# Performance work log

Measured on AMD Instinct MI355X. Metric: run time of the kernel, lower is better.

## Reference

```python
import jax, jax.numpy as jnp
import numpy as np

NUM_CLASSES = 9
TEMP = 0.1
ALPHA = 0.99
EPS = 1e-12  # F.normalize default eps


def _l2norm(x, axis=-1):
    n = jnp.linalg.norm(x, axis=axis, keepdims=True)
    return x / jnp.maximum(n, EPS)


def setup_inputs() -> dict:
    key = jax.random.key(0)
    k1, k2, k3, k4, k5 = jax.random.split(key, 5)
    B, D, h, w = 4, 768, 128, 128
    return {
        "cls_score": jax.random.normal(k1, (B, NUM_CLASSES, h, w), dtype=jnp.float32),
        "label": jax.random.randint(k2, (B, 4 * h, 4 * w), 0, NUM_CLASSES, dtype=jnp.int64),
        "gt_lucas": jax.random.randint(k3, (B, 4 * h, 4 * w), 0, NUM_CLASSES, dtype=jnp.int64),
        "features": jax.random.normal(k4, (B, D, h, w), dtype=jnp.float32),
        "prototypes": jax.random.uniform(k5, (NUM_CLASSES, D), dtype=jnp.float32),
    }


def reference(cls_score, label, gt_lucas, features, prototypes):
    B, D, h, w = features.shape
    # so the masked gathers reduce to a full flatten (static shapes).
    corine = label[:, ::4, ::4].reshape(-1)          # [N]
    lucas = gt_lucas[:, ::4, ::4].reshape(-1)        # [N] (mask trivially all valid)
    feats = jnp.transpose(features, (0, 2, 3, 1)).reshape(-1, D)  # [N, D]
    N = feats.shape[0]
    # note: original indexes corine labels under the lucas mask (mask all-true here)
    labels_lucas = corine
    labels_corine = jnp.where(corine == 7, 6, corine)
    # per-class EMA prototype update (unique(labels_lucas) == arange(9) by construction;
    # compute_ema detaches the new mean)
    sums = jax.ops.segment_sum(feats, labels_lucas, num_segments=NUM_CLASSES)      # [C, D]
    counts = jax.ops.segment_sum(jnp.ones((N,), feats.dtype), labels_lucas,
                                 num_segments=NUM_CLASSES)                          # [C]
    means = jax.lax.stop_gradient(sums / counts[:, None])
    protos = ALPHA * means + (1.0 - ALPHA) * prototypes
    protos = _l2norm(protos, axis=-1)                # F.normalize over feature dim
    logits = protos @ feats.T                        # [C, N]
    prot_feat = _l2norm(logits, axis=-1) / TEMP      # normalize each class row over N
    prot_feat = prot_feat.at[2].set((labels_corine == 2).astype(prot_feat.dtype))
    E = jnp.exp(prot_feat)                           # [C, N]
    A1 = E[labels_corine, jnp.arange(N)]             # [N]
    A2 = E.sum(axis=0)                               # [N]
    return jnp.mean(-jnp.log(A1 / A2))
```

## Files before the change

kernel.cpp:

```cpp
#include <hip/hip_runtime.h>
#include <math.h>

#define NCLS 9
#define DIM 768
#define NPIX 65536

#define OFF_LAB     ((size_t)0)
#define OFF_HIST    ((size_t)65536)
#define OFF_SUMS    ((size_t)74752)
#define OFF_SUMSQ   ((size_t)102400)
#define OFF_LOSS    ((size_t)102464)
#define OFF_DONE    ((size_t)102480)
#define OFF_LOGITS  ((size_t)139392)

__device__ __forceinline__ float waveReduceSum(float v) {
#pragma unroll
  for (int off = 32; off > 0; off >>= 1) v += __shfl_down(v, off, 64);
  return v;
}

__global__ void k0_lab(const int* __restrict__ label, unsigned char* __restrict__ lab,
                       int* __restrict__ hist, float* __restrict__ sumsq,
                       float* __restrict__ lossacc, unsigned int* __restrict__ done) {
  __shared__ int h[NCLS];
  int tid = threadIdx.x;
  if (tid < NCLS) h[tid] = 0;
  __syncthreads();
  int n = blockIdx.x * 256 + tid;
  int b = n >> 14, r = (n >> 7) & 127, cc = n & 127;
  int c = label[b * 262144 + r * 2048 + cc * 4];
  lab[n] = (unsigned char)c;
  atomicAdd(&h[c], 1);
  if (blockIdx.x == 0) {
    if (tid < 16) sumsq[tid] = 0.f;
    else if (tid == 16) lossacc[0] = 0.f;
    else if (tid == 17) done[0] = 0u;
  }
  __syncthreads();
  if (tid < NCLS) hist[blockIdx.x * NCLS + tid] = h[tid];
}

__global__ void k1_segsum(const float4* __restrict__ feat4, const uchar4* __restrict__ lab4,
                          float* __restrict__ sums) {
  int d = blockIdx.x;
  int tid = threadIdx.x;
  float acc[NCLS];
#pragma unroll
  for (int k = 0; k < NCLS; ++k) acc[k] = 0.f;
  for (int b = 0; b < 4; ++b) {
    const float4* fp = feat4 + (size_t)(b * DIM + d) * 4096;
    const uchar4* lp = lab4 + b * 4096;
#pragma unroll 4
    for (int i = 0; i < 16; ++i) {
      int p = tid + i * 256;
      float4 f = fp[p];
      uchar4 l = lp[p];
      int lx = l.x, ly = l.y, lz = l.z, lw = l.w;
#pragma unroll
      for (int k = 0; k < NCLS; ++k) {
        acc[k] += (lx == k) ? f.x : 0.f;
        acc[k] += (ly == k) ? f.y : 0.f;
        acc[k] += (lz == k) ? f.z : 0.f;
        acc[k] += (lw == k) ? f.w : 0.f;
      }
    }
  }
  __shared__ float red[4][NCLS];
#pragma unroll
  for (int k = 0; k < NCLS; ++k) acc[k] = waveReduceSum(acc[k]);
  int lane = tid & 63, w = tid >> 6;
  if (lane == 0) {
#pragma unroll
    for (int k = 0; k < NCLS; ++k) red[w][k] = acc[k];
  }
  __syncthreads();
  if (tid < NCLS)
    sums[tid * DIM + d] = red[0][tid] + red[1][tid] + red[2][tid] + red[3][tid];
}

__global__ void __launch_bounds__(1024, 8) k3_fused(const float* __restrict__ sums,
                                                    const int* __restrict__ hist,
                                                    const float* __restrict__ proto,
                                                    const float* __restrict__ feat,
                                                    float* __restrict__ logits,
                                                    float* __restrict__ sumsq) {
  __shared__ float pl[DIM * 12];
  __shared__ float cpart[32][NCLS];
  __shared__ float cnt[NCLS];
  __shared__ float red12[12][NCLS];
  __shared__ float invn[NCLS];
  __shared__ float red2[2][NCLS];
  int tid = threadIdx.x;

  if (tid < 288) {
    int c = tid % NCLS, g = tid / NCLS;
    int s = 0;
#pragma unroll
    for (int j = 0; j < 8; ++j) s += hist[(g * 8 + j) * NCLS + c];
    cpart[g][c] = (float)s;
  }
  __syncthreads();
  if (tid < NCLS) {
    float s = 0.f;
#pragma unroll
    for (int g = 0; g < 32; ++g) s += cpart[g][tid];
    cnt[tid] = s;
  }
  __syncthreads();

  float v[NCLS];
  if (tid < DIM) {
#pragma unroll
    for (int c = 0; c < NCLS; ++c)
      v[c] = 0.99f * (sums[c * DIM + tid] / cnt[c]) + 0.01f * proto[c * DIM + tid];
    int lane = tid & 63, w = tid >> 6;
#pragma unroll
    for (int c = 0; c < NCLS; ++c) {
      float q = waveReduceSum(v[c] * v[c]);
      if (lane == 0) red12[w][c] = q;
    }
  }
  __syncthreads();
  if (tid < NCLS) {
    float t = 0.f;
#pragma unroll
    for (int w2 = 0; w2 < 12; ++w2) t += red12[w2][tid];
    invn[tid] = 1.f / fmaxf(sqrtf(t), 1e-12f);
  }
  __syncthreads();
  if (tid < DIM) {
#pragma unroll
    for (int c = 0; c < NCLS; ++c) pl[tid * 12 + c] = v[c] * invn[c];
  }
  __syncthreads();

  int grp = tid >> 7, g = tid & 127;
  int n0 = blockIdx.x * 256;
  int b = n0 >> 14, ppb = n0 & 16383;
  const float* fr = feat + ((size_t)(b * DIM + grp * 96)) * 16384 + ppb + g;
  const float* pp = pl + (size_t)grp * 96 * 12;
  float a[NCLS][2];
#pragma unroll
  for (int c = 0; c < NCLS; ++c) { a[c][0] = 0.f; a[c][1] = 0.f; }

#pragma unroll 2
  for (int dd = 0; dd < 96; ++dd) {
    float f0 = fr[0], f1 = fr[128];
    float4 q0 = *(const float4*)pp;
    float4 q1 = *(const float4*)(pp + 4);
    float q8 = pp[8];
    float pcs[NCLS] = {q0.x, q0.y, q0.z, q0.w, q1.x, q1.y, q1.z, q1.w, q8};
#pragma unroll
    for (int c = 0; c < NCLS; ++c) {
      a[c][0] += pcs[c] * f0;
      a[c][1] += pcs[c] * f1;
    }
    fr += 16384;
    pp += 12;
  }
  __syncthreads();

  if (grp >= 4) {
    float* rp = pl + (size_t)(grp - 4) * 2304 + g;
#pragma unroll
    for (int c = 0; c < NCLS; ++c) {
      rp[c * 256] = a[c][0];
      rp[c * 256 + 128] = a[c][1];
    }
  }
  __syncthreads();
  if (grp < 4) {
    const float* rp = pl + (size_t)grp * 2304 + g;
#pragma unroll
    for (int c = 0; c < NCLS; ++c) {
      a[c][0] += rp[c * 256];
      a[c][1] += rp[c * 256 + 128];
    }
  }
  __syncthreads();
  if (grp >= 1 && grp < 4) {
    float* rp = pl + (size_t)(grp - 1) * 2304 + g;
#pragma unroll
    for (int c = 0; c < NCLS; ++c) {
      rp[c * 256] = a[c][0];
      rp[c * 256 + 128] = a[c][1];
    }
  }
  __syncthreads();
  if (grp == 0) {
#pragma unroll
    for (int q = 0; q < 3; ++q) {
      const float* rp = pl + (size_t)q * 2304 + g;
#pragma unroll
      for (int c = 0; c < NCLS; ++c) {
        a[c][0] += rp[c * 256];
        a[c][1] += rp[c * 256 + 128];
      }
    }
    float ss[NCLS];
#pragma unroll
    for (int c = 0; c < NCLS; ++c) {
      logits[(size_t)c * NPIX + n0 + g] = a[c][0];
      logits[(size_t)c * NPIX + n0 + 128 + g] = a[c][1];
      ss[c] = waveReduceSum(a[c][0] * a[c][0] + a[c][1] * a[c][1]);
    }
    int lane = tid & 63, w = tid >> 6;
    if (lane == 0) {
#pragma unroll
      for (int c = 0; c < NCLS; ++c) red2[w][c] = ss[c];
    }
  }
  __syncthreads();
  if (tid < NCLS) atomicAdd(&sumsq[tid], red2[0][tid] + red2[1][tid]);
}

__global__ void k5_loss(const float4* __restrict__ logits4, const uchar4* __restrict__ lab4,
                        const float* __restrict__ sumsq, float* __restrict__ lossacc,
                        unsigned int* __restrict__ done, float* __restrict__ out) {
  int t = blockIdx.x * 256 + threadIdx.x;
  int tid = threadIdx.x;
  float scale[NCLS];
#pragma unroll
  for (int c = 0; c < NCLS; ++c) scale[c] = 10.f / fmaxf(sqrtf(sumsq[c]), 1e-12f);
  float arr[NCLS][4];
#pragma unroll
  for (int c = 0; c < NCLS; ++c) {
    float4 v = logits4[(size_t)c * 16384 + t];
    arr[c][0] = v.x; arr[c][1] = v.y; arr[c][2] = v.z; arr[c][3] = v.w;
  }
  uchar4 lb = lab4[t];
  int lv[4] = {lb.x, lb.y, lb.z, lb.w};
  float lsum = 0.f;
#pragma unroll
  for (int j = 0; j < 4; ++j) {
    int l = lv[j];
    int lc = (l == 7) ? 6 : l;
    float sumE = 0.f, picked = 0.f;
#pragma unroll
    for (int c = 0; c < NCLS; ++c) {
      float pf = (c == 2) ? ((lc == 2) ? 1.f : 0.f) : arr[c][j] * scale[c];
      sumE += __expf(pf);
      picked += (c == lc) ? pf : 0.f;
    }
    lsum += __logf(sumE) - picked;
  }
  lsum = waveReduceSum(lsum);
  __shared__ float red[4];
  int lane = tid & 63, w = tid >> 6;
  if (lane == 0) red[w] = lsum;
  __syncthreads();
  if (tid == 0) {
    atomicAdd(lossacc, red[0] + red[1] + red[2] + red[3]);
    __threadfence();
    unsigned int ticket = atomicAdd(done, 1u);
    if (ticket == gridDim.x - 1) {
      __threadfence();
      float total = __hip_atomic_load(lossacc, __ATOMIC_ACQUIRE, __HIP_MEMORY_SCOPE_AGENT);
      out[0] = total * (1.f / (float)NPIX);
    }
  }
}

extern "C" void kernel_launch(void* const* d_in, const int* in_sizes, int n_in,
                              void* d_out, int out_size, void* d_ws, size_t ws_size,
                              hipStream_t stream) {
  const int* label = (const int*)d_in[1];
  const float* feat = (const float*)d_in[3];
  const float* proto = (const float*)d_in[4];
  char* ws = (char*)d_ws;
  unsigned char* lab = (unsigned char*)(ws + OFF_LAB);
  int* hist = (int*)(ws + OFF_HIST);
  float* sums = (float*)(ws + OFF_SUMS);
  float* sumsq = (float*)(ws + OFF_SUMSQ);
  float* lossacc = (float*)(ws + OFF_LOSS);
  unsigned int* done = (unsigned int*)(ws + OFF_DONE);
  float* logits = (float*)(ws + OFF_LOGITS);

  k0_lab<<<NPIX / 256, 256, 0, stream>>>(label, lab, hist, sumsq, lossacc, done);
  k1_segsum<<<DIM, 256, 0, stream>>>((const float4*)feat, (const uchar4*)lab, sums);
  k3_fused<<<NPIX / 256, 1024, 0, stream>>>(sums, hist, proto, feat, logits, sumsq);
  k5_loss<<<64, 256, 0, stream>>>((const float4*)logits, (const uchar4*)lab, sumsq, lossacc,
                                  done, (float*)d_out);
}
```

Baseline: 102.0 us.

## Split prototype normalization into a single-block kernel and read protos from global

The prototype EMA and L2 normalization used to be recomputed redundantly in each of the 256 blocks of the fused logits kernel. That work now runs once in a single-block kernel that writes a transposed, normalized prototype table to the workspace. The logits kernel reads prototypes directly from global or cache with a wave-uniform group index, and its unroll factor goes from 2 to 4. The cost is an extra kernel launch plus a serialized single-block step, and per-iteration prototype reads now go to global memory instead of LDS.

Result: slower. 110.0 us (+7.9%).

```diff
diff --git a/kernel.cpp b/kernel.cpp
--- a/kernel.cpp
+++ b/kernel.cpp
@@ -11,6 +11,7 @@
 #define OFF_SUMSQ   ((size_t)102400)
 #define OFF_LOSS    ((size_t)102464)
 #define OFF_DONE    ((size_t)102480)
+#define OFF_PROTO   ((size_t)102528)
 #define OFF_LOGITS  ((size_t)139392)
 
 __device__ __forceinline__ float waveReduceSum(float v) {
@@ -78,72 +79,68 @@
     sums[tid * DIM + d] = red[0][tid] + red[1][tid] + red[2][tid] + red[3][tid];
 }
 
-__global__ void __launch_bounds__(1024, 8) k3_fused(const float* __restrict__ sums,
-                                                    const int* __restrict__ hist,
-                                                    const float* __restrict__ proto,
-                                                    const float* __restrict__ feat,
-                                                    float* __restrict__ logits,
-                                                    float* __restrict__ sumsq) {
-  __shared__ float pl[DIM * 12];
-  __shared__ float cpart[32][NCLS];
+__global__ void k2_proto(const float* __restrict__ sums, const int* __restrict__ hist,
+                         const float* __restrict__ proto, float* __restrict__ protoT) {
+  __shared__ float red[12][NCLS];
+  __shared__ float inv[NCLS];
+  __shared__ float cpart[16][NCLS];
   __shared__ float cnt[NCLS];
-  __shared__ float red12[12][NCLS];
-  __shared__ float invn[NCLS];
-  __shared__ float red2[2][NCLS];
-  int tid = threadIdx.x;
-
-  if (tid < 288) {
+  int tid = threadIdx.x;
+  if (tid < 144) {
     int c = tid % NCLS, g = tid / NCLS;
     int s = 0;
 #pragma unroll
-    for (int j = 0; j < 8; ++j) s += hist[(g * 8 + j) * NCLS + c];
+    for (int j = 0; j < 16; ++j) s += hist[(g * 16 + j) * NCLS + c];
     cpart[g][c] = (float)s;
   }
   __syncthreads();
   if (tid < NCLS) {
     float s = 0.f;
 #pragma unroll
-    for (int g = 0; g < 32; ++g) s += cpart[g][tid];
+    for (int g = 0; g < 16; ++g) s += cpart[g][tid];
     cnt[tid] = s;
   }
   __syncthreads();
-
   float v[NCLS];
-  if (tid < DIM) {
-#pragma unroll
-    for (int c = 0; c < NCLS; ++c)
-      v[c] = 0.99f * (sums[c * DIM + tid] / cnt[c]) + 0.01f * proto[c * DIM + tid];
-    int lane = tid & 63, w = tid >> 6;
-#pragma unroll
-    for (int c = 0; c < NCLS; ++c) {
-      float q = waveReduceSum(v[c] * v[c]);
-      if (lane == 0) red12[w][c] = q;
-    }
+#pragma unroll
+  for (int c = 0; c < NCLS; ++c)
+    v[c] = 0.99f * (sums[c * DIM + tid] / cnt[c]) + 0.01f * proto[c * DIM + tid];
+  int lane = tid & 63, w = tid >> 6;
+#pragma unroll
+  for (int c = 0; c < NCLS; ++c) {
+    float q = waveReduceSum(v[c] * v[c]);
+    if (lane == 0) red[w][c] = q;
   }
   __syncthreads();
   if (tid < NCLS) {
     float t = 0.f;
 #pragma unroll
-    for (int w2 = 0; w2 < 12; ++w2) t += red12[w2][tid];
-    invn[tid] = 1.f / fmaxf(sqrtf(t), 1e-12f);
-  }
-  __syncthreads();
-  if (tid < DIM) {
-#pragma unroll
-    for (int c = 0; c < NCLS; ++c) pl[tid * 12 + c] = v[c] * invn[c];
-  }
-  __syncthreads();
-
-  int grp = tid >> 7, g = tid & 127;
+    for (int w2 = 0; w2 < 12; ++w2) t += red[w2][tid];
+    inv[tid] = 1.f / fmaxf(sqrtf(t), 1e-12f);
+  }
+  __syncthreads();
+#pragma unroll
+  for (int c = 0; c < NCLS; ++c) protoT[tid * 12 + c] = v[c] * inv[c];
+}
+
+__global__ void __launch_bounds__(1024) k3_logits(const float* __restrict__ feat,
+                                                  const float* __restrict__ protoT,
+                                                  float* __restrict__ logits,
+                                                  float* __restrict__ sumsq) {
+  __shared__ float pl[4 * 2304];
+  __shared__ float red2[2][NCLS];
+  int tid = threadIdx.x;
+  int grp = __builtin_amdgcn_readfirstlane(tid >> 7);
+  int g = tid & 127;
   int n0 = blockIdx.x * 256;
   int b = n0 >> 14, ppb = n0 & 16383;
   const float* fr = feat + ((size_t)(b * DIM + grp * 96)) * 16384 + ppb + g;
-  const float* pp = pl + (size_t)grp * 96 * 12;
+  const float* pp = protoT + grp * 96 * 12;
   float a[NCLS][2];
 #pragma unroll
   for (int c = 0; c < NCLS; ++c) { a[c][0] = 0.f; a[c][1] = 0.f; }
 
-#pragma unroll 2
+#pragma unroll 4
   for (int dd = 0; dd < 96; ++dd) {
     float f0 = fr[0], f1 = fr[128];
     float4 q0 = *(const float4*)pp;
@@ -274,11 +271,13 @@
   float* sumsq = (float*)(ws + OFF_SUMSQ);
   float* lossacc = (float*)(ws + OFF_LOSS);
   unsigned int* done = (unsigned int*)(ws + OFF_DONE);
+  float* protoT = (float*)(ws + OFF_PROTO);
   float* logits = (float*)(ws + OFF_LOGITS);
 
   k0_lab<<<NPIX / 256, 256, 0, stream>>>(label, lab, hist, sumsq, lossacc, done);
   k1_segsum<<<DIM, 256, 0, stream>>>((const float4*)feat, (const uchar4*)lab, sums);
-  k3_fused<<<NPIX / 256, 1024, 0, stream>>>(sums, hist, proto, feat, logits, sumsq);
+  k2_proto<<<1, 768, 0, stream>>>(sums, hist, proto, protoT);
+  k3_logits<<<NPIX / 256, 1024, 0, stream>>>(feat, protoT, logits, sumsq);
   k5_loss<<<64, 256, 0, stream>>>((const float4*)logits, (const uchar4*)lab, sumsq, lossacc,
                                   done, (float*)d_out);
 }
```
